# Performance work log

Hardware: AMD Instinct MI355X
Metric: run time of the kernel (lower is better)

The kernel has to match this reference:

```python
import jax, jax.numpy as jnp
import numpy as np

B, L, D = 2, 2048, 2048
NH, NKV = 16, 8
HD = D // NH            # 128
GQ = NH // NKV          # queries per kv head
THETA = 10000.0
SCALE = HD ** -0.5


def rope_tables(seq_len, dim, theta):
    inv_freq = 1.0 / theta ** (jnp.arange(0, dim, 2, dtype=jnp.float32) / dim)
    t = jnp.arange(seq_len, dtype=jnp.float32)
    freqs = jnp.outer(t, inv_freq)              # [L, dim/2]
    emb = jnp.concatenate([freqs, freqs], -1)   # [L, dim]
    return jnp.cos(emb), jnp.sin(emb)


def rotate_half(x):
    x1, x2 = jnp.split(x, 2, axis=-1)
    return jnp.concatenate([-x2, x1], -1)


def setup_inputs() -> dict:
    key = jax.random.key(0)
    ks = jax.random.split(key, 5)
    s = 0.02
    return {
        "x": jax.random.normal(ks[0], (B, L, D), jnp.float32),
        "Wq": jax.random.normal(ks[1], (NH * HD, D), jnp.float32) * s,
        "Wk": jax.random.normal(ks[2], (NKV * HD, D), jnp.float32) * s,
        "Wv": jax.random.normal(ks[3], (NKV * HD, D), jnp.float32) * s,
        "Wo": jax.random.normal(ks[4], (D, D), jnp.float32) * s,
    }


def reference(x, Wq, Wk, Wv, Wo):
    b, l, d = x.shape
    q = (x @ Wq.T).reshape(b, l, NH, HD).transpose(0, 2, 1, 3)    # [B,NH,L,HD]
    k = (x @ Wk.T).reshape(b, l, NKV, HD).transpose(0, 2, 1, 3)   # [B,NKV,L,HD]
    v = (x @ Wv.T).reshape(b, l, NKV, HD).transpose(0, 2, 1, 3)

    cos, sin = rope_tables(l, HD, THETA)                           # [L,HD]
    q = q * cos + rotate_half(q) * sin
    k = k * cos + rotate_half(k) * sin

    # GQA without materializing expanded K/V: group queries per kv head
    qg = q.reshape(b, NKV, GQ, l, HD)
    scores = jnp.einsum('bgrld,bgmd->bgrlm', qg, k) * SCALE        # [B,NKV,GQ,L,L]
    causal = jnp.triu(jnp.ones((l, l), bool), k=1)
    scores = jnp.where(causal, -jnp.inf, scores)
    attn = jax.nn.softmax(scores.astype(jnp.float32), axis=-1).astype(q.dtype)
    out = jnp.einsum('bgrlm,bgmd->bgrld', attn, v)                 # [B,NKV,GQ,L,HD]
    out = out.reshape(b, NH, l, HD).transpose(0, 2, 1, 3).reshape(b, l, d)
    return out @ Wo.T
```

## Files before the change

### kernel.cpp

```cpp
#include <hip/hip_runtime.h>
#include <cmath>

using u16 = unsigned short;
typedef u16    u16x4  __attribute__((ext_vector_type(4)));
typedef u16    u16x8  __attribute__((ext_vector_type(8)));
typedef __bf16 bf16x8 __attribute__((ext_vector_type(8)));
typedef float  f32x4  __attribute__((ext_vector_type(4)));

constexpr int Bc  = 2;
constexpr int Lc  = 2048;
constexpr int Dc  = 2048;
constexpr int NHc = 16;
constexpr int NKVc= 8;
constexpr int HDc = 128;

__device__ __forceinline__ u16 f2b(float f) {
  union { float f; unsigned u; } v; v.f = f;
  unsigned r = v.u + 0x7FFFu + ((v.u >> 16) & 1u);
  return (u16)(r >> 16);
}
__device__ __forceinline__ u16 f2b_fast(float f) {
  union { float f; unsigned u; } v; v.f = f;
  return (u16)((v.u + 0x8000u) >> 16);
}
__device__ __forceinline__ float b2f(u16 s) {
  union { unsigned u; float f; } v; v.u = ((unsigned)s) << 16;
  return v.f;
}
__device__ __forceinline__ bf16x8 ld_frag(const u16* p) {
  u16x8 u = *(const u16x8*)p;
  return __builtin_bit_cast(bf16x8, u);
}
__device__ __forceinline__ void gld_lds16(u16* ldst, const u16* gsrc) {
  __builtin_amdgcn_global_load_lds(
      (const __attribute__((address_space(1))) void*)gsrc,
      (__attribute__((address_space(3))) void*)ldst, 16, 0, 0);
}

__global__ void cvt_f32_bf16(const float* __restrict__ src, u16* __restrict__ dst, int n) {
  int i = (blockIdx.x * blockDim.x + threadIdx.x) * 4;
  if (i >= n) return;
  float4 v = *(const float4*)&src[i];
  u16x4 o = { f2b(v.x), f2b(v.y), f2b(v.z), f2b(v.w) };
  *(u16x4*)&dst[i] = o;
}

__global__ void cvt_w3(const float* __restrict__ Wq, const float* __restrict__ Wk,
                       const float* __restrict__ Wv, u16* __restrict__ dst) {
  const int n1 = Dc * Dc;
  const int n2 = n1 + (NKVc*HDc) * Dc;
  const int n3 = n2 + (NKVc*HDc) * Dc;
  int i = (blockIdx.x * blockDim.x + threadIdx.x) * 4;
  if (i >= n3) return;
  const float* src; int off;
  if (i < n1)      { src = Wq; off = i; }
  else if (i < n2) { src = Wk; off = i - n1; }
  else             { src = Wv; off = i - n2; }
  float4 v = *(const float4*)&src[off];
  u16x4 o = { f2b(v.x), f2b(v.y), f2b(v.z), f2b(v.w) };
  *(u16x4*)&dst[i] = o;
}

#define MFMA_(a, b, c) __builtin_amdgcn_mfma_f32_16x16x32_bf16(a, b, c, 0, 0, 0)
#define BAR()   __builtin_amdgcn_s_barrier()
#define LGKM0() { __asm__ volatile("s_waitcnt lgkmcnt(0)" ::: "memory"); \
                  __builtin_amdgcn_sched_barrier(0); }
#define PRIO1() __builtin_amdgcn_s_setprio(1)
#define PRIO0() __builtin_amdgcn_s_setprio(0)

#define STG(lb, gp, goff, h, kc)                                          \
  { _Pragma("unroll")                                                     \
    for (int i_ = 0; i_ < 2; ++i_) {                                      \
      int c_ = wave + (i_ << 3);                                          \
      gld_lds16((lb) + (h) * 8192 + c_ * 512,                             \
                (gp) + (goff) + (size_t)(h) * 262144 + (size_t)c_ * 16384 + (kc)); } }

#define LDA_(bA, mi, kk) ld_frag((bA) + ((wm << 7) + ((mi) << 4) + l16) * 64 + \
                                 (((quad + ((kk) << 2)) ^ t7) << 3))
#define LDB_(bB, ni, kk) ld_frag((bB) + ((wn << 6) + ((ni) << 4) + l16) * 64 + \
                                 (((quad + ((kk) << 2)) ^ t7) << 3))

#define QUAD_MFMA(MI0, NI0, BARR)                                                      \
  { _Pragma("unroll")                                                                  \
    for (int mi_ = 0; mi_ < 4; ++mi_) {                                                \
      _Pragma("unroll")                                                                \
      for (int ni_ = 0; ni_ < 2; ++ni_) {                                              \
        acc[(MI0)+mi_][(NI0)+ni_] =                                                    \
            MFMA_(aF[mi_][0], BARR[ni_][0], acc[(MI0)+mi_][(NI0)+ni_]);                \
        acc[(MI0)+mi_][(NI0)+ni_] =                                                    \
            MFMA_(aF[mi_][1], BARR[ni_][1], acc[(MI0)+mi_][(NI0)+ni_]); } } }

__global__ __launch_bounds__(512, 2) void gemm256_qkv(
    const u16* __restrict__ A, const u16* __restrict__ W,
    u16* __restrict__ Qp, u16* __restrict__ Kp, u16* __restrict__ Vtp)
{
  __shared__ u16 lds[65536];
  const int tid  = threadIdx.x;
  const int wave = tid >> 6, lane = tid & 63;
  const int quad = lane >> 4, l16 = lane & 15, t7 = l16 & 7;
  const int bid = blockIdx.x;
  const int swz = (bid & 7) * 32 + (bid >> 3);
  const int tx = swz & 15, ty = swz >> 4;
  const int m0 = ty * 256, n0 = tx * 256;
  const int wm = wave >> 2, wn = wave & 3;
  const int srow = lane >> 3;
  const int sx8  = ((lane & 7) ^ srow) << 3;

  u16* const A0L = lds;
  u16* const B0L = lds + 16384;
  u16* const A1L = lds + 32768;
  u16* const B1L = lds + 49152;

  const size_t aOff = (size_t)(m0 + srow) * 2048 + sx8;
  const size_t bOff = (size_t)(n0 + srow) * 2048 + sx8;

  f32x4 acc[8][4];
#pragma unroll
  for (int i = 0; i < 8; ++i)
#pragma unroll
    for (int j = 0; j < 4; ++j) acc[i][j] = {0.f, 0.f, 0.f, 0.f};
  bf16x8 aF[4][2], bL[2][2], bH[2][2];

  STG(A0L, A, aOff, 0, 0);  STG(A0L, A, aOff, 1, 0);
  STG(B0L, W, bOff, 0, 0);  STG(B0L, W, bOff, 1, 0);
  STG(B1L, W, bOff, 0, 64); STG(B1L, W, bOff, 1, 64);
  __asm__ volatile("s_waitcnt vmcnt(4)" ::: "memory");
  BAR();

  int kc = 0;
  for (int it = 0; it < 16; ++it, kc += 128) {
    const bool st2 = (it < 15);
#pragma unroll
    for (int mi = 0; mi < 4; ++mi) { aF[mi][0] = LDA_(A0L, mi, 0); aF[mi][1] = LDA_(A0L, mi, 1); }
#pragma unroll
    for (int ni = 0; ni < 2; ++ni) { bL[ni][0] = LDB_(B0L, ni, 0); bL[ni][1] = LDB_(B0L, ni, 1); }
    STG(A1L, A, aOff, 0, kc + 64);
    __asm__ volatile("s_waitcnt lgkmcnt(8)" ::: "memory");
    BAR(); LGKM0(); PRIO1();
    QUAD_MFMA(0, 0, bL);
    PRIO0(); BAR();
#pragma unroll
    for (int ni = 0; ni < 2; ++ni) { bH[ni][0] = LDB_(B0L, 2 + ni, 0); bH[ni][1] = LDB_(B0L, 2 + ni, 1); }
    STG(A1L, A, aOff, 1, kc + 64);
    BAR(); LGKM0(); PRIO1();
    QUAD_MFMA(0, 2, bH);
    PRIO0(); BAR();
#pragma unroll
    for (int mi = 0; mi < 4; ++mi) { aF[mi][0] = LDA_(A0L, 4 + mi, 0); aF[mi][1] = LDA_(A0L, 4 + mi, 1); }
    if (st2) STG(B0L, W, bOff, 0, kc + 128);
    BAR(); LGKM0(); PRIO1();
    QUAD_MFMA(4, 0, bL);
    PRIO0(); BAR();
    if (st2) STG(B0L, W, bOff, 1, kc + 128);
    BAR(); PRIO1();
    QUAD_MFMA(4, 2, bH);
    PRIO0();
    if (st2) { __asm__ volatile("s_waitcnt vmcnt(4)" ::: "memory"); }
    else     { __asm__ volatile("s_waitcnt vmcnt(0)" ::: "memory"); }
    BAR();
#pragma unroll
    for (int mi = 0; mi < 4; ++mi) { aF[mi][0] = LDA_(A1L, mi, 0); aF[mi][1] = LDA_(A1L, mi, 1); }
#pragma unroll
    for (int ni = 0; ni < 2; ++ni) { bL[ni][0] = LDB_(B1L, ni, 0); bL[ni][1] = LDB_(B1L, ni, 1); }
    if (st2) STG(A0L, A, aOff, 0, kc + 128);
    __asm__ volatile("s_waitcnt lgkmcnt(8)" ::: "memory");
    BAR(); LGKM0(); PRIO1();
    QUAD_MFMA(0, 0, bL);
    PRIO0(); BAR();
#pragma unroll
    for (int ni = 0; ni < 2; ++ni) { bH[ni][0] = LDB_(B1L, 2 + ni, 0); bH[ni][1] = LDB_(B1L, 2 + ni, 1); }
    if (st2) STG(A0L, A, aOff, 1, kc + 128);
    BAR(); LGKM0(); PRIO1();
    QUAD_MFMA(0, 2, bH);
    PRIO0(); BAR();
#pragma unroll
    for (int mi = 0; mi < 4; ++mi) { aF[mi][0] = LDA_(A1L, 4 + mi, 0); aF[mi][1] = LDA_(A1L, 4 + mi, 1); }
    if (st2) STG(B1L, W, bOff, 0, kc + 192);
    BAR(); LGKM0(); PRIO1();
    QUAD_MFMA(4, 0, bL);
    PRIO0(); BAR();
    if (st2) STG(B1L, W, bOff, 1, kc + 192);
    BAR(); PRIO1();
    QUAD_MFMA(4, 2, bH);
    PRIO0();
    if (st2) { __asm__ volatile("s_waitcnt vmcnt(4)" ::: "memory"); }
    BAR();
  }

  if (n0 < 3072) {
    u16* Cb; int ldc, nc0;
    if (n0 < 2048) { Cb = Qp; ldc = 2048; nc0 = n0; }
    else           { Cb = Kp; ldc = 1024; nc0 = n0 - 2048; }
#pragma unroll
    for (int mi = 0; mi < 8; ++mi)
#pragma unroll
      for (int ni = 0; ni < 4; ++ni)
#pragma unroll
        for (int r = 0; r < 4; ++r) {
          int m = m0 + wm * 128 + mi * 16 + quad * 4 + r;
          int n = nc0 + wn * 64 + ni * 16 + l16;
          Cb[(size_t)m * ldc + n] = f2b(acc[mi][ni][r]);
        }
  } else {
    __syncthreads();
#pragma unroll
    for (int mi = 0; mi < 8; ++mi)
#pragma unroll
      for (int ni = 0; ni < 4; ++ni)
#pragma unroll
        for (int r = 0; r < 4; ++r) {
          int l = wm * 128 + mi * 16 + quad * 4 + r;
          int d = wn * 64 + ni * 16 + l16;
          lds[l * 256 + (((d >> 3) ^ (l & 31)) << 3) + (d & 7)] = f2b(acc[mi][ni][r]);
        }
    __syncthreads();
    const int b    = m0 >> 11;
    const int hkv0 = (n0 - 3072) >> 7;
#pragma unroll
    for (int it2 = 0; it2 < 16; ++it2) {
      int sl = tid + it2 * 512;
      int dl = sl >> 5;
      int lc = (sl & 31) * 8;
      u16x8 v;
#pragma unroll
      for (int e = 0; e < 8; ++e) {
        int l = lc + e;
        v[e] = lds[l * 256 + (((dl >> 3) ^ (l & 31)) << 3) + (dl & 7)];
      }
      const int hkv = hkv0 + (dl >> 7);
      const int d   = dl & 127;
      *(u16x8*)&Vtp[(((size_t)b * NKVc + hkv) * HDc + d) * (size_t)Lc + (m0 & (Lc - 1)) + lc] = v;
    }
  }
}
#undef STG
#undef LDA_
#undef LDB_
#undef QUAD_MFMA

__global__ __launch_bounds__(256) void gemm_out(
    const u16* __restrict__ A, const u16* __restrict__ W,
    float* __restrict__ Cf, int M, int N, int K)
{
  __shared__ u16 lds[16384];
  u16* lA = lds;
  u16* lB = lds + 8192;
  const int tid  = threadIdx.x;
  const int wave = tid >> 6, lane = tid & 63;
  const int quad = lane >> 4, l16 = lane & 15;
  const int t7   = l16 & 7;
  const int m0 = blockIdx.y * 128, n0 = blockIdx.x * 128;
  const int mw = (wave >> 1) * 64, nw = (wave & 1) * 64;
  const int r8 = lane >> 3;
  const int cgl = (lane & 7) ^ r8;

  f32x4 acc[4][4];
#pragma unroll
  for (int i = 0; i < 4; ++i)
#pragma unroll
    for (int j = 0; j < 4; ++j) acc[i][j] = {0.f, 0.f, 0.f, 0.f};

  for (int kt = 0; kt < K; kt += 64) {
#pragma unroll
    for (int cc = 0; cc < 4; ++cc) {
      int c = wave + cc * 4;
      gld_lds16(&lA[c * 512], &A[(size_t)(m0 + 8 * c + r8) * K + kt + cgl * 8]);
      gld_lds16(&lB[c * 512], &W[(size_t)(n0 + 8 * c + r8) * K + kt + cgl * 8]);
    }
    __syncthreads();
#pragma unroll
    for (int s = 0; s < 2; ++s) {
      bf16x8 af[4], bf[4];
#pragma unroll
      for (int i = 0; i < 4; ++i)
        af[i] = ld_frag(&lA[(mw + i*16 + l16) * 64 + ((quad + 4*s) ^ t7) * 8]);
#pragma unroll
      for (int j = 0; j < 4; ++j)
        bf[j] = ld_frag(&lB[(nw + j*16 + l16) * 64 + ((quad + 4*s) ^ t7) * 8]);
#pragma unroll
      for (int i = 0; i < 4; ++i)
#pragma unroll
        for (int j = 0; j < 4; ++j)
          acc[i][j] = __builtin_amdgcn_mfma_f32_16x16x32_bf16(af[i], bf[j], acc[i][j], 0, 0, 0);
    }
    __syncthreads();
  }

#pragma unroll
  for (int i = 0; i < 4; ++i)
#pragma unroll
    for (int j = 0; j < 4; ++j)
#pragma unroll
      for (int r = 0; r < 4; ++r) {
        int m = m0 + mw + i*16 + quad*4 + r;
        int n = n0 + nw + j*16 + l16;
        Cf[(size_t)m * N + n] = acc[i][j][r];
      }
}

__global__ void rope2_kernel(u16* __restrict__ Qp, u16* __restrict__ Kp, float qs)
{
  const int nQ = Bc * Lc * NHc * 64;
  const int nT = nQ + Bc * Lc * NKVc * 64;
  int t = blockIdx.x * blockDim.x + threadIdx.x;
  if (t >= nT) return;
  u16* T; int nheads; float osc; int idx;
  if (t < nQ) { T = Qp; nheads = NHc;  osc = qs;  idx = t; }
  else        { T = Kp; nheads = NKVc; osc = 1.f; idx = t - nQ; }
  int d   = idx & 63;
  int h   = (idx >> 6) % nheads;
  int row = idx / (nheads * 64);
  int l   = row & (Lc - 1);
  float freq = exp2f((float)d * (-13.287712379549449f / 64.f));
  float ang  = (float)l * freq;
  float s, c;
  sincosf(ang, &s, &c);
  size_t base = (size_t)row * (nheads * 128) + h * 128;
  float x1 = b2f(T[base + d]);
  float x2 = b2f(T[base + d + 64]);
  T[base + d]      = f2b((x1 * c - x2 * s) * osc);
  T[base + d + 64] = f2b((x2 * c + x1 * s) * osc);
}

__global__ __launch_bounds__(512) void flash_kernel(
    const u16* __restrict__ Q, const u16* __restrict__ K, const u16* __restrict__ Vt,
    u16* __restrict__ O)
{
  __shared__ u16 smem[41984];
  const int tid  = threadIdx.x;
  const int wave = tid >> 6, lane = tid & 63;
  const int quad = lane >> 4, l16 = lane & 15;
  const int hw = wave >> 2, wr = wave & 3;
  const int bhkv = blockIdx.x;
  const int b = bhkv >> 3, hkv = bhkv & 7;
  const int h = hkv * 2 + hw;

  const size_t kbase = ((size_t)b * Lc) * (NKVc * HDc) + (size_t)hkv * HDc;
  const size_t vbase = (((size_t)b * NKVc + hkv) * HDc) * (size_t)Lc;

  const int kr8 = lane >> 4;
  const int kcl = lane & 15;
  const int vr16 = lane >> 3;
  const int vkl  = lane & 7;

  u16* sP_w = smem + 32768 + wave * 1152;

  for (int pass = 0; pass < 2; ++pass) {
    const int qt = (pass == 0) ? (31 - (int)blockIdx.y) : (int)blockIdx.y;
    const int q0 = qt * 64;

    __syncthreads();
#pragma unroll
    for (int i = 0; i < 4; ++i) {
      int g = tid + i * 512;
      int row = g >> 4, cg = g & 15;
      int qh = hkv * 2 + (row >> 6);
      int rr = row & 63;
      *(u16x8*)&smem[row * 128 + (cg ^ (row & 15)) * 8] =
          *(const u16x8*)&Q[((size_t)(b * Lc + q0 + rr)) * Dc + (size_t)qh * HDc + cg * 8];
    }
    __syncthreads();
    bf16x8 qf[4];
#pragma unroll
    for (int ks = 0; ks < 4; ++ks)
      qf[ks] = ld_frag(&smem[(hw*64 + wr*16 + l16) * 128 + ((ks*4 + quad) ^ l16) * 8]);
    __syncthreads();

#pragma unroll
    for (int i = 0; i < 2; ++i) {
      int c = wave + i * 8;
      int row = c * 4 + kr8;
      gld_lds16(smem + c * 512,
                &K[kbase + (size_t)row * (NKVc*HDc) + (size_t)(kcl ^ (row & 15)) * 8]);
    }
#pragma unroll
    for (int i = 0; i < 2; ++i) {
      int c = wave + i * 8;
      int d = c * 8 + vr16;
      gld_lds16(smem + 16384 + c * 512,
                &Vt[vbase + (size_t)d * Lc + (size_t)(vkl ^ (d & 7)) * 8]);
    }

    f32x4 acc_o[8];
#pragma unroll
    for (int i = 0; i < 8; ++i) acc_o[i] = {0.f, 0.f, 0.f, 0.f};
    float ps[4] = {0.f, 0.f, 0.f, 0.f};

    for (int kt = 0; kt <= qt; ++kt) {
      const int kOff  = (kt & 1) ? 8192 : 0;
      const int kOffN = (kt & 1) ? 0 : 8192;
      const int vOff  = (kt & 1) ? 24576 : 16384;
      const int vOffN = (kt & 1) ? 16384 : 24576;

      __asm__ volatile("s_waitcnt vmcnt(2)\n\ts_barrier" ::: "memory");

      if (kt < qt) {
#pragma unroll
        for (int i = 0; i < 2; ++i) {
          int c = wave + i * 8;
          int row = (kt + 1) * 64 + c * 4 + kr8;
          gld_lds16(smem + kOffN + c * 512,
                    &K[kbase + (size_t)row * (NKVc*HDc) + (size_t)(kcl ^ (row & 15)) * 8]);
        }
      }

      const u16* sKc = smem + kOff;
      f32x4 accs[4];
#pragma unroll
      for (int n = 0; n < 4; ++n) accs[n] = {0.f, 0.f, 0.f, 0.f};
#pragma unroll
      for (int ks = 0; ks < 4; ++ks)
#pragma unroll
        for (int n = 0; n < 4; ++n) {
          bf16x8 kf = ld_frag(&sKc[(n*16 + l16) * 128 + ((ks*4 + quad) ^ l16) * 8]);
          accs[n] = __builtin_amdgcn_mfma_f32_16x16x32_bf16(qf[ks], kf, accs[n], 0, 0, 0);
        }

      const int qrow = q0 + wr*16 + quad*4;
      if (kt == qt) {
#pragma unroll
        for (int n = 0; n < 4; ++n) {
          int kg = kt*64 + n*16 + l16;
#pragma unroll
          for (int r = 0; r < 4; ++r)
            if (kg > qrow + r) accs[n][r] = -INFINITY;
        }
      }
#pragma unroll
      for (int n = 0; n < 4; ++n)
#pragma unroll
        for (int r = 0; r < 4; ++r) {
          float p = exp2f(accs[n][r]);
          accs[n][r] = p;
          ps[r] += p;
        }

#pragma unroll
      for (int n = 0; n < 4; ++n)
#pragma unroll
        for (int r = 0; r < 4; ++r)
          sP_w[(quad*4 + r) * 72 + n*16 + l16] = f2b_fast(accs[n][r]);

      if (kt < qt)
        __asm__ volatile("s_waitcnt vmcnt(2) lgkmcnt(0)\n\ts_barrier" ::: "memory");
      else
        __asm__ volatile("s_waitcnt vmcnt(0) lgkmcnt(0)\n\ts_barrier" ::: "memory");

      if (kt < qt) {
#pragma unroll
        for (int i = 0; i < 2; ++i) {
          int c = wave + i * 8;
          int d = c * 8 + vr16;
          gld_lds16(smem + vOffN + c * 512,
                    &Vt[vbase + (size_t)d * Lc + (kt+1)*64 + (size_t)(vkl ^ (d & 7)) * 8]);
        }
      }

      const u16* sVc = smem + vOff;
#pragma unroll
      for (int s2 = 0; s2 < 2; ++s2) {
        bf16x8 pf = ld_frag(&sP_w[l16 * 72 + s2*32 + quad*8]);
#pragma unroll
        for (int di = 0; di < 8; ++di) {
          bf16x8 vf = ld_frag(&sVc[(di*16 + l16) * 64 + ((s2*4 + quad) ^ (l16 & 7)) * 8]);
          acc_o[di] = __builtin_amdgcn_mfma_f32_16x16x32_bf16(pf, vf, acc_o[di], 0, 0, 0);
        }
      }
    }

#pragma unroll
    for (int off = 1; off < 16; off <<= 1)
#pragma unroll
      for (int r = 0; r < 4; ++r) ps[r] += __shfl_xor(ps[r], off);
    float inv[4];
#pragma unroll
    for (int r = 0; r < 4; ++r) inv[r] = 1.0f / ps[r];

#pragma unroll
    for (int di = 0; di < 8; ++di)
#pragma unroll
      for (int r = 0; r < 4; ++r) {
        int qrow = q0 + wr*16 + quad*4 + r;
        int d = di*16 + l16;
        float v = acc_o[di][r] * inv[r];
        O[((size_t)(b * Lc + qrow)) * Dc + (size_t)h * HDc + d] = f2b(v);
      }
  }
}

extern "C" void kernel_launch(void* const* d_in, const int* in_sizes, int n_in,
                              void* d_out, int out_size, void* d_ws, size_t ws_size,
                              hipStream_t stream)
{
  const float* x  = (const float*)d_in[0];
  const float* Wq = (const float*)d_in[1];
  const float* Wk = (const float*)d_in[2];
  const float* Wv = (const float*)d_in[3];
  const float* Wo = (const float*)d_in[4];
  float* out = (float*)d_out;

  const int M = Bc * Lc;
  u16* ws = (u16*)d_ws;
  u16* xb   = ws;
  u16* Ow   = xb;
  u16* Wcat = ws + (size_t)8 * 1024 * 1024;
  u16* Wob  = Wcat;
  u16* Qw   = Wcat + (size_t)8 * 1024 * 1024;
  u16* Kw   = Qw   + (size_t)8 * 1024 * 1024;
  u16* Vt   = Kw   + (size_t)4 * 1024 * 1024;

  const int nx = M * Dc;
  const int nq = Dc * Dc;
  const int nw3 = nq + 2 * (NKVc*HDc) * Dc;
  cvt_f32_bf16<<<nx/1024, 256, 0, stream>>>(x, xb, nx);
  cvt_w3<<<nw3/1024, 256, 0, stream>>>(Wq, Wk, Wv, Wcat);

  gemm256_qkv<<<256, 512, 0, stream>>>(xb, Wcat, Qw, Kw, Vt);

  const float qs = 0.08838834764831845f * 1.4426950408889634f;
  const int nrope = M * (NHc + NKVc) * 64;
  rope2_kernel<<<(nrope + 255) / 256, 256, 0, stream>>>(Qw, Kw, qs);

  flash_kernel<<<dim3(Bc*NKVc, 16), 512, 0, stream>>>(Qw, Kw, Vt, Ow);

  cvt_f32_bf16<<<nq/1024, 256, 0, stream>>>(Wo, Wob, nq);
  gemm_out<<<dim3(16, 32), 256, 0, stream>>>(Ow, Wob, out, M, Dc, Dc);
}
```

Measured before the change: 339.4 us.

## Software-pipeline QKV GEMM LDS fragment reads one phase ahead of MFMAs

```diff
diff --git a/kernel.cpp b/kernel.cpp
--- a/kernel.cpp
+++ b/kernel.cpp
@@ -63,8 +63,12 @@
 
 #define MFMA_(a, b, c) __builtin_amdgcn_mfma_f32_16x16x32_bf16(a, b, c, 0, 0, 0)
 #define BAR()   __builtin_amdgcn_s_barrier()
+#define SB0()   __builtin_amdgcn_sched_barrier(0)
 #define LGKM0() { __asm__ volatile("s_waitcnt lgkmcnt(0)" ::: "memory"); \
                   __builtin_amdgcn_sched_barrier(0); }
+#define VMC4()  __asm__ volatile("s_waitcnt vmcnt(4)" ::: "memory")
+#define VMC2()  __asm__ volatile("s_waitcnt vmcnt(2)" ::: "memory")
+#define VMC0()  __asm__ volatile("s_waitcnt vmcnt(0)" ::: "memory")
 #define PRIO1() __builtin_amdgcn_s_setprio(1)
 #define PRIO0() __builtin_amdgcn_s_setprio(0)
 
@@ -75,20 +79,31 @@
       gld_lds16((lb) + (h) * 8192 + c_ * 512,                             \
                 (gp) + (goff) + (size_t)(h) * 262144 + (size_t)c_ * 16384 + (kc)); } }
 
-#define LDA_(bA, mi, kk) ld_frag((bA) + ((wm << 7) + ((mi) << 4) + l16) * 64 + \
-                                 (((quad + ((kk) << 2)) ^ t7) << 3))
-#define LDB_(bB, ni, kk) ld_frag((bB) + ((wn << 6) + ((ni) << 4) + l16) * 64 + \
-                                 (((quad + ((kk) << 2)) ^ t7) << 3))
-
-#define QUAD_MFMA(MI0, NI0, BARR)                                                      \
-  { _Pragma("unroll")                                                                  \
-    for (int mi_ = 0; mi_ < 4; ++mi_) {                                                \
-      _Pragma("unroll")                                                                \
-      for (int ni_ = 0; ni_ < 2; ++ni_) {                                              \
-        acc[(MI0)+mi_][(NI0)+ni_] =                                                    \
-            MFMA_(aF[mi_][0], BARR[ni_][0], acc[(MI0)+mi_][(NI0)+ni_]);                \
-        acc[(MI0)+mi_][(NI0)+ni_] =                                                    \
-            MFMA_(aF[mi_][1], BARR[ni_][1], acc[(MI0)+mi_][(NI0)+ni_]); } } }
+#define RD_ALO(rp) { _Pragma("unroll") for (int mi_ = 0; mi_ < 4; ++mi_) { \
+    aLo[mi_][0] = ld_frag((rp) + mi_*1024 + cg0);                          \
+    aLo[mi_][1] = ld_frag((rp) + mi_*1024 + cg1); } }
+#define RD_AHI01(rp) { _Pragma("unroll") for (int mi_ = 0; mi_ < 2; ++mi_) { \
+    aHi[mi_][0] = ld_frag((rp) + (4+mi_)*1024 + cg0);                        \
+    aHi[mi_][1] = ld_frag((rp) + (4+mi_)*1024 + cg1); } }
+#define RD_AHI23(rp) { _Pragma("unroll") for (int mi_ = 0; mi_ < 2; ++mi_) { \
+    aHi[2+mi_][0] = ld_frag((rp) + (6+mi_)*1024 + cg0);                      \
+    aHi[2+mi_][1] = ld_frag((rp) + (6+mi_)*1024 + cg1); } }
+#define RD_BLO(rp) { _Pragma("unroll") for (int ni_ = 0; ni_ < 2; ++ni_) { \
+    bLo[ni_][0] = ld_frag((rp) + ni_*1024 + cg0);                          \
+    bLo[ni_][1] = ld_frag((rp) + ni_*1024 + cg1); } }
+#define RD_BHI(rp) { _Pragma("unroll") for (int ni_ = 0; ni_ < 2; ++ni_) { \
+    bHi[ni_][0] = ld_frag((rp) + (2+ni_)*1024 + cg0);                      \
+    bHi[ni_][1] = ld_frag((rp) + (2+ni_)*1024 + cg1); } }
+
+#define QMFMA(MI0, NI0, AX, BX)                                                \
+  { _Pragma("unroll")                                                          \
+    for (int mi_ = 0; mi_ < 4; ++mi_) {                                        \
+      _Pragma("unroll")                                                        \
+      for (int ni_ = 0; ni_ < 2; ++ni_) {                                      \
+        acc[(MI0)+mi_][(NI0)+ni_] =                                            \
+            MFMA_(AX[mi_][0], BX[ni_][0], acc[(MI0)+mi_][(NI0)+ni_]);          \
+        acc[(MI0)+mi_][(NI0)+ni_] =                                            \
+            MFMA_(AX[mi_][1], BX[ni_][1], acc[(MI0)+mi_][(NI0)+ni_]); } } }
 
 __global__ __launch_bounds__(512, 2) void gemm256_qkv(
     const u16* __restrict__ A, const u16* __restrict__ W,
@@ -114,77 +129,55 @@
   const size_t aOff = (size_t)(m0 + srow) * 2048 + sx8;
   const size_t bOff = (size_t)(n0 + srow) * 2048 + sx8;
 
+  const int cg0 = ((quad ^ t7) << 3);
+  const int cg1 = (((quad ^ t7) ^ 4) << 3);
+  const u16* const rA0 = A0L + wm * 8192 + l16 * 64;
+  const u16* const rA1 = A1L + wm * 8192 + l16 * 64;
+  const u16* const rB0 = B0L + wn * 4096 + l16 * 64;
+  const u16* const rB1 = B1L + wn * 4096 + l16 * 64;
+
   f32x4 acc[8][4];
 #pragma unroll
   for (int i = 0; i < 8; ++i)
 #pragma unroll
     for (int j = 0; j < 4; ++j) acc[i][j] = {0.f, 0.f, 0.f, 0.f};
-  bf16x8 aF[4][2], bL[2][2], bH[2][2];
+  bf16x8 aLo[4][2], aHi[4][2], bLo[2][2], bHi[2][2];
 
   STG(A0L, A, aOff, 0, 0);  STG(A0L, A, aOff, 1, 0);
   STG(B0L, W, bOff, 0, 0);  STG(B0L, W, bOff, 1, 0);
-  STG(B1L, W, bOff, 0, 64); STG(B1L, W, bOff, 1, 64);
-  __asm__ volatile("s_waitcnt vmcnt(4)" ::: "memory");
+  STG(A1L, A, aOff, 0, 64); STG(A1L, A, aOff, 1, 64);
+  VMC4();
   BAR();
-
-  int kc = 0;
-  for (int it = 0; it < 16; ++it, kc += 128) {
-    const bool st2 = (it < 15);
-#pragma unroll
-    for (int mi = 0; mi < 4; ++mi) { aF[mi][0] = LDA_(A0L, mi, 0); aF[mi][1] = LDA_(A0L, mi, 1); }
-#pragma unroll
-    for (int ni = 0; ni < 2; ++ni) { bL[ni][0] = LDB_(B0L, ni, 0); bL[ni][1] = LDB_(B0L, ni, 1); }
-    STG(A1L, A, aOff, 0, kc + 64);
-    __asm__ volatile("s_waitcnt lgkmcnt(8)" ::: "memory");
-    BAR(); LGKM0(); PRIO1();
-    QUAD_MFMA(0, 0, bL);
-    PRIO0(); BAR();
-#pragma unroll
-    for (int ni = 0; ni < 2; ++ni) { bH[ni][0] = LDB_(B0L, 2 + ni, 0); bH[ni][1] = LDB_(B0L, 2 + ni, 1); }
-    STG(A1L, A, aOff, 1, kc + 64);
-    BAR(); LGKM0(); PRIO1();
-    QUAD_MFMA(0, 2, bH);
-    PRIO0(); BAR();
-#pragma unroll
-    for (int mi = 0; mi < 4; ++mi) { aF[mi][0] = LDA_(A0L, 4 + mi, 0); aF[mi][1] = LDA_(A0L, 4 + mi, 1); }
-    if (st2) STG(B0L, W, bOff, 0, kc + 128);
-    BAR(); LGKM0(); PRIO1();
-    QUAD_MFMA(4, 0, bL);
-    PRIO0(); BAR();
-    if (st2) STG(B0L, W, bOff, 1, kc + 128);
-    BAR(); PRIO1();
-    QUAD_MFMA(4, 2, bH);
-    PRIO0();
-    if (st2) { __asm__ volatile("s_waitcnt vmcnt(4)" ::: "memory"); }
-    else     { __asm__ volatile("s_waitcnt vmcnt(0)" ::: "memory"); }
-    BAR();
-#pragma unroll
-    for (int mi = 0; mi < 4; ++mi) { aF[mi][0] = LDA_(A1L, mi, 0); aF[mi][1] = LDA_(A1L, mi, 1); }
-#pragma unroll
-    for (int ni = 0; ni < 2; ++ni) { bL[ni][0] = LDB_(B1L, ni, 0); bL[ni][1] = LDB_(B1L, ni, 1); }
-    if (st2) STG(A0L, A, aOff, 0, kc + 128);
-    __asm__ volatile("s_waitcnt lgkmcnt(8)" ::: "memory");
-    BAR(); LGKM0(); PRIO1();
-    QUAD_MFMA(0, 0, bL);
-    PRIO0(); BAR();
-#pragma unroll
-    for (int ni = 0; ni < 2; ++ni) { bH[ni][0] = LDB_(B1L, 2 + ni, 0); bH[ni][1] = LDB_(B1L, 2 + ni, 1); }
-    if (st2) STG(A0L, A, aOff, 1, kc + 128);
-    BAR(); LGKM0(); PRIO1();
-    QUAD_MFMA(0, 2, bH);
-    PRIO0(); BAR();
-#pragma unroll
-    for (int mi = 0; mi < 4; ++mi) { aF[mi][0] = LDA_(A1L, 4 + mi, 0); aF[mi][1] = LDA_(A1L, 4 + mi, 1); }
-    if (st2) STG(B1L, W, bOff, 0, kc + 192);
-    BAR(); LGKM0(); PRIO1();
-    QUAD_MFMA(4, 0, bL);
-    PRIO0(); BAR();
-    if (st2) STG(B1L, W, bOff, 1, kc + 192);
-    BAR(); PRIO1();
-    QUAD_MFMA(4, 2, bH);
-    PRIO0();
-    if (st2) { __asm__ volatile("s_waitcnt vmcnt(4)" ::: "memory"); }
-    BAR();
+  RD_ALO(rA0); RD_BLO(rB0);
+  LGKM0();
+
+  for (int it = 0; it < 16; ++it) {
+    const int t2 = it * 128;
+    const bool g = (it < 15);
+    RD_BHI(rB0); RD_AHI01(rA0);
+    STG(B1L, W, bOff, 0, t2 + 64);
+    SB0(); PRIO1(); QMFMA(0, 0, aLo, bLo); PRIO0(); LGKM0(); BAR();
+    RD_AHI23(rA0);
+    STG(B1L, W, bOff, 1, t2 + 64);
+    VMC4();
+    SB0(); PRIO1(); QMFMA(0, 2, aLo, bHi); PRIO0(); LGKM0(); BAR();
+    RD_ALO(rA1);
+    if (g) { STG(A0L, A, aOff, 0, t2 + 128); VMC2(); }
+    else   { VMC0(); }
+    SB0(); PRIO1(); QMFMA(4, 0, aHi, bLo); PRIO0(); LGKM0(); BAR();
+    RD_BLO(rB1);
+    if (g) STG(A0L, A, aOff, 1, t2 + 128);
+    SB0(); PRIO1(); QMFMA(4, 2, aHi, bHi); PRIO0(); LGKM0(); BAR();
+    RD_BHI(rB1); RD_AHI01(rA1);
+    if (g) STG(B0L, W, bOff, 0, t2 + 128);
+    SB0(); PRIO1(); QMFMA(0, 0, aLo, bLo); PRIO0(); LGKM0(); BAR();
+    RD_AHI23(rA1);
+    if (g) { STG(B0L, W, bOff, 1, t2 + 128); VMC4(); }
+    SB0(); PRIO1(); QMFMA(0, 2, aLo, bHi); PRIO0(); LGKM0(); BAR();
+    if (g) { RD_ALO(rA0); STG(A1L, A, aOff, 0, t2 + 192); VMC2(); }
+    SB0(); PRIO1(); QMFMA(4, 0, aHi, bLo); PRIO0(); LGKM0(); BAR();
+    if (g) { RD_BLO(rB0); STG(A1L, A, aOff, 1, t2 + 192); }
+    SB0(); PRIO1(); QMFMA(4, 2, aHi, bHi); PRIO0(); LGKM0(); BAR();
   }
 
   if (n0 < 3072) {
@@ -211,7 +204,8 @@
         for (int r = 0; r < 4; ++r) {
           int l = wm * 128 + mi * 16 + quad * 4 + r;
           int d = wn * 64 + ni * 16 + l16;
-          lds[l * 256 + (((d >> 3) ^ (l & 31)) << 3) + (d & 7)] = f2b(acc[mi][ni][r]);
+          int cgp = ((d >> 3) ^ (l & 31) ^ (l >> 5)) & 31;
+          lds[l * 256 + (cgp << 3) + (d & 7)] = f2b(acc[mi][ni][r]);
         }
     __syncthreads();
     const int b    = m0 >> 11;
@@ -225,7 +219,8 @@
 #pragma unroll
       for (int e = 0; e < 8; ++e) {
         int l = lc + e;
-        v[e] = lds[l * 256 + (((dl >> 3) ^ (l & 31)) << 3) + (dl & 7)];
+        int cgp = ((dl >> 3) ^ (l & 31) ^ (l >> 5)) & 31;
+        v[e] = lds[l * 256 + (cgp << 3) + (dl & 7)];
       }
       const int hkv = hkv0 + (dl >> 7);
       const int d   = dl & 127;
@@ -234,9 +229,12 @@
   }
 }
 #undef STG
-#undef LDA_
-#undef LDB_
-#undef QUAD_MFMA
+#undef RD_ALO
+#undef RD_AHI01
+#undef RD_AHI23
+#undef RD_BLO
+#undef RD_BHI
+#undef QMFMA
 
 __global__ __launch_bounds__(256) void gemm_out(
     const u16* __restrict__ A, const u16* __restrict__ W,
```

Measured after the change: 314.5 us. -7.3%, faster.
